# Kernel tuning notes

Measured on AMD Instinct MI355X. Metric: run time of the kernel, lower is better.

## Reference

```python
import jax, jax.numpy as jnp
import numpy as np

B, T, D, H = 4, 2048, 1024, 16
HD = D // H  # 64


def setup_inputs() -> dict:
    key = jax.random.key(0)
    ks = jax.random.split(key, 9)
    s = 1.0 / np.sqrt(D)
    return {
        "x": jax.random.normal(ks[0], (B, T, D), dtype=jnp.float32),
        "Wq": jax.random.normal(ks[1], (D, D), dtype=jnp.float32) * s,
        "bq": jnp.zeros((D,), dtype=jnp.float32),
        "Wk": jax.random.normal(ks[2], (D, D), dtype=jnp.float32) * s,
        "bk": jnp.zeros((D,), dtype=jnp.float32),
        "Wv": jax.random.normal(ks[3], (D, D), dtype=jnp.float32) * s,
        "bv": jnp.zeros((D,), dtype=jnp.float32),
        "Wo": jax.random.normal(ks[4], (D, D), dtype=jnp.float32) * s,
        "bo": jnp.zeros((D,), dtype=jnp.float32),
    }


def reference(x, Wq, bq, Wk, bk, Wv, bv, Wo, bo):
    Bx, Tx, C = x.shape
    # QKV projections -> (B, H, T, HD)
    q = (x @ Wq + bq).reshape(Bx, Tx, H, HD).transpose(0, 2, 1, 3)
    k = (x @ Wk + bk).reshape(Bx, Tx, H, HD).transpose(0, 2, 1, 3)
    v = (x @ Wv + bv).reshape(Bx, Tx, H, HD).transpose(0, 2, 1, 3)
    # scaled dot-product scores (B, H, T, T)
    scores = jnp.einsum("bhqd,bhkd->bhqk", q, k) / jnp.sqrt(jnp.float32(HD))
    causal = jnp.tril(jnp.ones((Tx, Tx), dtype=bool))
    scores = jnp.where(causal[None, None, :, :], scores, jnp.float32(-1e9))
    attn = jax.nn.softmax(scores, axis=-1)
    out = jnp.einsum("bhqk,bhkd->bhqd", attn, v)  # (B, H, T, HD)
    out = out.transpose(0, 2, 1, 3).reshape(Bx, Tx, C)
    return out @ Wo + bo
```

## Files before the change

### kernel.cpp

```cpp
#include <hip/hip_runtime.h>


#define B_  4
#define T_  2048
#define D_  1024
#define H_  16
#define HD_ 64
#define M_  (B_ * T_)

typedef __bf16 bf16x8 __attribute__((ext_vector_type(8)));
typedef float  floatx4 __attribute__((ext_vector_type(4)));

__device__ __forceinline__ unsigned short f2b(float f) {
  unsigned int u = __float_as_uint(f);
  unsigned int r = (u + 0x7fffu + ((u >> 16) & 1u)) >> 16;
  return (unsigned short)r;
}

__device__ __forceinline__ float fast_exp2(float x) {
#if __has_builtin(__builtin_amdgcn_exp2f)
  return __builtin_amdgcn_exp2f(x);
#else
  return exp2f(x);
#endif
}

__device__ __forceinline__ void async_ld16(const void* g, void* l) {
  __builtin_amdgcn_global_load_lds(
      (const __attribute__((address_space(1))) void*)g,
      (__attribute__((address_space(3))) void*)l, 16, 0, 0);
}


__global__ void cast_fp32_to_bf16(const float* __restrict__ in,
                                  unsigned short* __restrict__ out, int n) {
  int i = (blockIdx.x * 256 + threadIdx.x) * 4;
  if (i >= n) return;
  float4 v = *(const float4*)(in + i);
  ushort4 o;
  o.x = f2b(v.x); o.y = f2b(v.y); o.z = f2b(v.z); o.w = f2b(v.w);
  *(ushort4*)(out + i) = o;
}

__global__ void transpose_cast(const float* __restrict__ W0, const float* __restrict__ W1,
                               const float* __restrict__ W2, const float* __restrict__ W3,
                               unsigned short* __restrict__ O0, unsigned short* __restrict__ O1,
                               unsigned short* __restrict__ O2, unsigned short* __restrict__ O3) {
  __shared__ float tile[32][33];
  int z = blockIdx.z;
  const float* W = z == 0 ? W0 : z == 1 ? W1 : z == 2 ? W2 : W3;
  unsigned short* O = z == 0 ? O0 : z == 1 ? O1 : z == 2 ? O2 : O3;
  int n0 = blockIdx.x * 32, k0 = blockIdx.y * 32;
  int tx = threadIdx.x, ty = threadIdx.y;
#pragma unroll
  for (int i = 0; i < 4; ++i)
    tile[ty + i * 8][tx] = W[(size_t)(k0 + ty + i * 8) * D_ + n0 + tx];
  __syncthreads();
#pragma unroll
  for (int i = 0; i < 4; ++i)
    O[(size_t)(n0 + ty + i * 8) * D_ + k0 + tx] = f2b(tile[tx][ty + i * 8]);
}


__global__ __launch_bounds__(256, 2)
void gemm_qkv(const unsigned short* __restrict__ A,
              const unsigned short* __restrict__ Wt,
              const float* __restrict__ bq, const float* __restrict__ bk,
              const float* __restrict__ bv,
              unsigned short* __restrict__ Qo, unsigned short* __restrict__ Ko,
              unsigned short* __restrict__ Vo) {
  __shared__ __align__(16) unsigned short As[128 * 64];
  __shared__ __align__(16) unsigned short Bs[128 * 64];
  const int K = D_;

  const int tid = threadIdx.x;
  const int wave = tid >> 6, lane = tid & 63;
  const int quad = lane >> 4, l16 = lane & 15;
  const int m0 = blockIdx.y * 128, n0 = blockIdx.x * 128;
  const int wm = (wave >> 1) * 64, wn = (wave & 1) * 64;

  const int rsub = lane >> 3;
  const int csw = ((lane & 7) ^ rsub) * 8;
  const int rw = wave * 32;

  const unsigned short* Ag = A + (size_t)(m0 + rw + rsub) * K + csw;
  const unsigned short* Bg = Wt + (size_t)(n0 + rw + rsub) * K + csw;

  floatx4 acc[4][4] = {};

  for (int kt = 0; kt < K; kt += 64) {
#pragma unroll
    for (int j = 0; j < 4; ++j) {
      async_ld16(Ag + (size_t)(j * 8) * K + kt, &As[(rw + j * 8) * 64]);
      async_ld16(Bg + (size_t)(j * 8) * K + kt, &Bs[(rw + j * 8) * 64]);
    }
    __syncthreads();

#pragma unroll
    for (int kk = 0; kk < 2; ++kk) {
      bf16x8 a[4], b[4];
#pragma unroll
      for (int i = 0; i < 4; ++i) {
        const int ra = wm + i * 16 + l16;
        a[i] = *(const bf16x8*)&As[ra * 64 + (((kk * 4 + quad) ^ (ra & 7)) * 8)];
      }
#pragma unroll
      for (int i = 0; i < 4; ++i) {
        const int rb = wn + i * 16 + l16;
        b[i] = *(const bf16x8*)&Bs[rb * 64 + (((kk * 4 + quad) ^ (rb & 7)) * 8)];
      }
#pragma unroll
      for (int mi = 0; mi < 4; ++mi)
#pragma unroll
        for (int ni = 0; ni < 4; ++ni)
          acc[mi][ni] = __builtin_amdgcn_mfma_f32_16x16x32_bf16(
              a[mi], b[ni], acc[mi][ni], 0, 0, 0);
    }
    __syncthreads();
  }

  const int which = n0 >> 10;
  const float* bias = which == 0 ? bq : which == 1 ? bk : bv;
  unsigned short* Out = which == 0 ? Qo : which == 1 ? Ko : Vo;

#pragma unroll
  for (int mi = 0; mi < 4; ++mi) {
#pragma unroll
    for (int ni = 0; ni < 4; ++ni) {
#pragma unroll
      for (int r = 0; r < 4; ++r) {
        const int m = m0 + wm + mi * 16 + quad * 4 + r;
        const int n = n0 + wn + ni * 16 + l16;
        const float val = acc[mi][ni][r] + bias[n & 1023];
        const int b = m >> 11, t = m & (T_ - 1);
        const int nl = n & 1023;
        const int h = nl >> 6, d = nl & (HD_ - 1);
        size_t idx;
        if (which == 2) {
          const int tp = (t & ~63) | (((t & 15) << 2) | ((t >> 4) & 3));
          idx = ((size_t)(b * H_ + h) * HD_ + d) * T_ + tp;
        } else {
          idx = ((size_t)(b * H_ + h) * T_ + t) * HD_ + d;
        }
        Out[idx] = f2b(val);
      }
    }
  }
}


__global__ __launch_bounds__(256, 2)
void gemm_out(const unsigned short* __restrict__ A,
              const unsigned short* __restrict__ Bt,
              const float* __restrict__ bias,
              float* __restrict__ Cout, int N, int K) {
  __shared__ __align__(16) unsigned short As[128 * 64];
  __shared__ __align__(16) unsigned short Bs[128 * 64];

  const int tid = threadIdx.x;
  const int wave = tid >> 6, lane = tid & 63;
  const int quad = lane >> 4, l16 = lane & 15;
  const int m0 = blockIdx.y * 128, n0 = blockIdx.x * 128;
  const int wm = (wave >> 1) * 64, wn = (wave & 1) * 64;

  const int rsub = lane >> 3;
  const int csw = ((lane & 7) ^ rsub) * 8;
  const int rw = wave * 32;

  const unsigned short* Ag = A + (size_t)(m0 + rw + rsub) * K + csw;
  const unsigned short* Bg = Bt + (size_t)(n0 + rw + rsub) * K + csw;

  floatx4 acc[4][4] = {};

  for (int kt = 0; kt < K; kt += 64) {
#pragma unroll
    for (int j = 0; j < 4; ++j) {
      async_ld16(Ag + (size_t)(j * 8) * K + kt, &As[(rw + j * 8) * 64]);
      async_ld16(Bg + (size_t)(j * 8) * K + kt, &Bs[(rw + j * 8) * 64]);
    }
    __syncthreads();

#pragma unroll
    for (int kk = 0; kk < 2; ++kk) {
      bf16x8 a[4], b[4];
#pragma unroll
      for (int i = 0; i < 4; ++i) {
        const int ra = wm + i * 16 + l16;
        a[i] = *(const bf16x8*)&As[ra * 64 + (((kk * 4 + quad) ^ (ra & 7)) * 8)];
      }
#pragma unroll
      for (int i = 0; i < 4; ++i) {
        const int rb = wn + i * 16 + l16;
        b[i] = *(const bf16x8*)&Bs[rb * 64 + (((kk * 4 + quad) ^ (rb & 7)) * 8)];
      }
#pragma unroll
      for (int mi = 0; mi < 4; ++mi)
#pragma unroll
        for (int ni = 0; ni < 4; ++ni)
          acc[mi][ni] = __builtin_amdgcn_mfma_f32_16x16x32_bf16(
              a[mi], b[ni], acc[mi][ni], 0, 0, 0);
    }
    __syncthreads();
  }

#pragma unroll
  for (int mi = 0; mi < 4; ++mi)
#pragma unroll
    for (int ni = 0; ni < 4; ++ni)
#pragma unroll
      for (int r = 0; r < 4; ++r) {
        const int m = m0 + wm + mi * 16 + quad * 4 + r;
        const int n = n0 + wn + ni * 16 + l16;
        Cout[(size_t)m * N + n] = acc[mi][ni][r] + bias[n];
      }
}


#define PSTR 72

template <bool MASKED>
__device__ __forceinline__ void attn_chunk(
    int kbse, int qw, int quad, int l16,
    const unsigned short* __restrict__ Ks,
    const unsigned short* __restrict__ Vs,
    const bf16x8 (&aq)[2][2], floatx4 (&o)[2][4], floatx4 (&lacc)[2],
    unsigned short* __restrict__ pl0, unsigned short* __restrict__ pl1,
    bf16x8 vones) {
  const int sw = l16 & 7;

  bf16x8 kf0[4], kf1[4];
#pragma unroll
  for (int j = 0; j < 4; ++j) {
    const unsigned short* kr = &Ks[(j * 16 + l16) * HD_];
    kf0[j] = *(const bf16x8*)&kr[(quad ^ sw) * 8];
    kf1[j] = *(const bf16x8*)&kr[((quad + 4) ^ sw) * 8];
  }

  floatx4 s[2][4] = {};
#pragma unroll
  for (int qt = 0; qt < 2; ++qt)
#pragma unroll
    for (int j = 0; j < 4; ++j) {
      s[qt][j] = __builtin_amdgcn_mfma_f32_16x16x32_bf16(aq[qt][0], kf0[j], s[qt][j], 0, 0, 0);
      s[qt][j] = __builtin_amdgcn_mfma_f32_16x16x32_bf16(aq[qt][1], kf1[j], s[qt][j], 0, 0, 0);
    }

  bf16x8 vf0[4], vf1[4];
#pragma unroll
  for (int d4 = 0; d4 < 4; ++d4) {
    const unsigned short* vr = &Vs[(d4 * 16 + l16) * 64];
    vf0[d4] = *(const bf16x8*)&vr[(quad ^ sw) * 8];
    vf1[d4] = *(const bf16x8*)&vr[((quad + 4) ^ sw) * 8];
  }

  const float SL = 0.125f * 1.44269504f;
  const float CB = 8.0f * 1.44269504f;
#pragma unroll
  for (int qt = 0; qt < 2; ++qt) {
    unsigned short* pw = qt ? pl1 : pl0;
#pragma unroll
    for (int r = 0; r < 4; ++r) {
      float v0 = s[qt][0][r], v1 = s[qt][1][r], v2 = s[qt][2][r], v3 = s[qt][3][r];
      if (MASKED) {
        const int qrow = qw + qt * 16 + quad * 4 + r;
        if (kbse + l16 > qrow)      v0 = -1e30f;
        if (kbse + 16 + l16 > qrow) v1 = -1e30f;
        if (kbse + 32 + l16 > qrow) v2 = -1e30f;
        if (kbse + 48 + l16 > qrow) v3 = -1e30f;
      }
      const float p0 = fast_exp2(__builtin_fmaf(v0, SL, -CB));
      const float p1 = fast_exp2(__builtin_fmaf(v1, SL, -CB));
      const float p2 = fast_exp2(__builtin_fmaf(v2, SL, -CB));
      const float p3 = fast_exp2(__builtin_fmaf(v3, SL, -CB));
      uint2 pk;
      pk.x = __builtin_amdgcn_perm(__float_as_uint(p1), __float_as_uint(p0), 0x07060302u);
      pk.y = __builtin_amdgcn_perm(__float_as_uint(p3), __float_as_uint(p2), 0x07060302u);
      *(uint2*)&pw[(quad * 4 + r) * PSTR + 4 * l16] = pk;
    }
  }

#pragma unroll
  for (int qt = 0; qt < 2; ++qt) {
    const unsigned short* pw = qt ? pl1 : pl0;
    const bf16x8 pf0 = *(const bf16x8*)&pw[l16 * PSTR + quad * 8];
    const bf16x8 pf1 = *(const bf16x8*)&pw[l16 * PSTR + 32 + quad * 8];
    lacc[qt] = __builtin_amdgcn_mfma_f32_16x16x32_bf16(pf0, vones, lacc[qt], 0, 0, 0);
    lacc[qt] = __builtin_amdgcn_mfma_f32_16x16x32_bf16(pf1, vones, lacc[qt], 0, 0, 0);
#pragma unroll
    for (int d4 = 0; d4 < 4; ++d4) {
      o[qt][d4] = __builtin_amdgcn_mfma_f32_16x16x32_bf16(pf0, vf0[d4], o[qt][d4], 0, 0, 0);
      o[qt][d4] = __builtin_amdgcn_mfma_f32_16x16x32_bf16(pf1, vf1[d4], o[qt][d4], 0, 0, 0);
    }
  }
}

__global__ __launch_bounds__(256, 2)
void attn_kernel(const unsigned short* __restrict__ Q,
                 const unsigned short* __restrict__ K,
                 const unsigned short* __restrict__ Vp,
                 unsigned short* __restrict__ O) {
  __shared__ __align__(16) unsigned short Ks[64 * HD_];
  __shared__ __align__(16) unsigned short Vs[HD_ * 64];
  __shared__ unsigned short Pl[4][2][16 * PSTR];

  const int bidx = blockIdx.x;
  const int xcd = bidx & 7;
  const int t = bidx >> 3;
  const int j = t >> 5;
  const int slot = t & 31;
  const int bh_local = slot >> 2;
  const int v = slot & 3;
  const int k4 = (j == 0) ? v : (j == 1) ? 15 - v : (j == 2) ? v + 4 : 11 - v;
  const int bh = (xcd << 3) | bh_local;

  const int wave = threadIdx.x >> 6, lane = threadIdx.x & 63;
  const int quad = lane >> 4, l16 = lane & 15;
  const int tile = k4 * 4 + wave;
  const int qw = tile * 32;

  const unsigned short* Qb = Q + (size_t)bh * T_ * HD_;
  const unsigned short* Kb = K + (size_t)bh * T_ * HD_;
  const unsigned short* Vb = Vp + (size_t)bh * HD_ * T_;

  bf16x8 aq[2][2];
#pragma unroll
  for (int qt = 0; qt < 2; ++qt) {
    const unsigned short* qp = Qb + (size_t)(qw + qt * 16 + l16) * HD_;
    aq[qt][0] = *(const bf16x8*)(qp + quad * 8);
    aq[qt][1] = *(const bf16x8*)(qp + 32 + quad * 8);
  }

  union { unsigned short u[8]; bf16x8 v8; } ones;
#pragma unroll
  for (int i = 0; i < 8; ++i) ones.u[i] = 0x3F80;

  floatx4 o[2][4] = {};
  floatx4 lacc[2] = {};

  const int rsub = lane >> 3;
  const int csw = ((lane & 7) ^ rsub) * 8;
  const int rA = 8 * wave;
  const int rB = 8 * (wave + 4);

  const int my_nfull = tile >> 1;
  const int nit = 2 * k4 + 2;

  for (int kc = 0; kc < nit; ++kc) {
    const int kbse = kc * 64;
    if (kc) __syncthreads();
    async_ld16(Kb + (size_t)(kbse + rA + rsub) * HD_ + csw, &Ks[rA * HD_]);
    async_ld16(Kb + (size_t)(kbse + rB + rsub) * HD_ + csw, &Ks[rB * HD_]);
    async_ld16(Vb + (size_t)(rA + rsub) * T_ + kbse + csw, &Vs[rA * 64]);
    async_ld16(Vb + (size_t)(rB + rsub) * T_ + kbse + csw, &Vs[rB * 64]);
    __syncthreads();

    if (kc < my_nfull)
      attn_chunk<false>(kbse, qw, quad, l16, Ks, Vs, aq, o, lacc,
                        &Pl[wave][0][0], &Pl[wave][1][0], ones.v8);
    else if (kc == my_nfull)
      attn_chunk<true>(kbse, qw, quad, l16, Ks, Vs, aq, o, lacc,
                       &Pl[wave][0][0], &Pl[wave][1][0], ones.v8);
  }

  const int b = bh >> 4, h = bh & 15;
#pragma unroll
  for (int qt = 0; qt < 2; ++qt) {
#pragma unroll
    for (int r = 0; r < 4; ++r) {
      const float inv = 1.0f / lacc[qt][r];
      const int tt = qw + qt * 16 + quad * 4 + r;
      unsigned short* orow = O + (size_t)(b * T_ + tt) * D_ + h * HD_;
      orow[l16]      = f2b(o[qt][0][r] * inv);
      orow[16 + l16] = f2b(o[qt][1][r] * inv);
      orow[32 + l16] = f2b(o[qt][2][r] * inv);
      orow[48 + l16] = f2b(o[qt][3][r] * inv);
    }
  }
}


extern "C" void kernel_launch(void* const* d_in, const int* in_sizes, int n_in,
                              void* d_out, int out_size, void* d_ws, size_t ws_size,
                              hipStream_t stream) {
  const float* x  = (const float*)d_in[0];
  const float* Wq = (const float*)d_in[1];
  const float* bq = (const float*)d_in[2];
  const float* Wk = (const float*)d_in[3];
  const float* bk = (const float*)d_in[4];
  const float* Wv = (const float*)d_in[5];
  const float* bv = (const float*)d_in[6];
  const float* Wo = (const float*)d_in[7];
  const float* bo = (const float*)d_in[8];
  float* out = (float*)d_out;

  char* ws = (char*)d_ws;
  const size_t MB = 1u << 20;
  unsigned short* xb  = (unsigned short*)(ws);
  unsigned short* Wqt = (unsigned short*)(ws + 16 * MB);
  unsigned short* Wkt = (unsigned short*)(ws + 18 * MB);
  unsigned short* Wvt = (unsigned short*)(ws + 20 * MB);
  unsigned short* Wot = (unsigned short*)(ws + 22 * MB);
  unsigned short* Qb  = (unsigned short*)(ws + 24 * MB);
  unsigned short* Kb  = (unsigned short*)(ws + 40 * MB);
  unsigned short* Vtb = (unsigned short*)(ws + 56 * MB);
  unsigned short* Ob  = xb;

  cast_fp32_to_bf16<<<dim3(M_ * D_ / 1024), dim3(256), 0, stream>>>(x, xb, M_ * D_);
  transpose_cast<<<dim3(32, 32, 4), dim3(32, 8), 0, stream>>>(
      Wq, Wk, Wv, Wo, Wqt, Wkt, Wvt, Wot);

  gemm_qkv<<<dim3(24, M_ / 128), dim3(256), 0, stream>>>(
      xb, Wqt, bq, bk, bv, Qb, Kb, Vtb);

  attn_kernel<<<dim3(1024), dim3(256), 0, stream>>>(Qb, Kb, Vtb, Ob);

  gemm_out<<<dim3(D_ / 128, M_ / 128), dim3(256), 0, stream>>>(
      Ob, Wot, bo, out, D_, D_);
}
```

Baseline: 259.6 us.

## Overlap next K/V tile load with softmax and PV compute in attention

Splits the attention chunk into a QK/V-fragment-load phase and a softmax+PV phase. After K and V fragments are pulled into registers, the single shared buffer is released and the async load for the next tile is issued, so global loads overlap the softmax and PV work. This keeps a single LDS buffer but holds V fragments in registers longer, which adds register pressure. Barriers per iteration stay at two.

After: 264.4 us. About the same (+1.8%).

```diff
diff --git a/kernel.cpp b/kernel.cpp
--- a/kernel.cpp
+++ b/kernel.cpp
@@ -218,14 +218,12 @@
 
 #define PSTR 72
 
-template <bool MASKED>
-__device__ __forceinline__ void attn_chunk(
-    int kbse, int qw, int quad, int l16,
+__device__ __forceinline__ void attn_qk(
+    int quad, int l16,
     const unsigned short* __restrict__ Ks,
     const unsigned short* __restrict__ Vs,
-    const bf16x8 (&aq)[2][2], floatx4 (&o)[2][4], floatx4 (&lacc)[2],
-    unsigned short* __restrict__ pl0, unsigned short* __restrict__ pl1,
-    bf16x8 vones) {
+    const bf16x8 (&aq)[2][2], floatx4 (&s)[2][4],
+    bf16x8 (&vf0)[4], bf16x8 (&vf1)[4]) {
   const int sw = l16 & 7;
 
   bf16x8 kf0[4], kf1[4];
@@ -236,7 +234,6 @@
     kf1[j] = *(const bf16x8*)&kr[((quad + 4) ^ sw) * 8];
   }
 
-  floatx4 s[2][4] = {};
 #pragma unroll
   for (int qt = 0; qt < 2; ++qt)
 #pragma unroll
@@ -245,14 +242,21 @@
       s[qt][j] = __builtin_amdgcn_mfma_f32_16x16x32_bf16(aq[qt][1], kf1[j], s[qt][j], 0, 0, 0);
     }
 
-  bf16x8 vf0[4], vf1[4];
 #pragma unroll
   for (int d4 = 0; d4 < 4; ++d4) {
     const unsigned short* vr = &Vs[(d4 * 16 + l16) * 64];
     vf0[d4] = *(const bf16x8*)&vr[(quad ^ sw) * 8];
     vf1[d4] = *(const bf16x8*)&vr[((quad + 4) ^ sw) * 8];
   }
-
+}
+
+template <bool MASKED>
+__device__ __forceinline__ void attn_sm_pv(
+    int kbse, int qw, int quad, int l16,
+    floatx4 (&s)[2][4], const bf16x8 (&vf0)[4], const bf16x8 (&vf1)[4],
+    floatx4 (&o)[2][4], floatx4 (&lacc)[2],
+    unsigned short* __restrict__ pl0, unsigned short* __restrict__ pl1,
+    bf16x8 vones) {
   const float SL = 0.125f * 1.44269504f;
   const float CB = 8.0f * 1.44269504f;
 #pragma unroll
@@ -345,21 +349,40 @@
   const int my_nfull = tile >> 1;
   const int nit = 2 * k4 + 2;
 
+  async_ld16(Kb + (size_t)(rA + rsub) * HD_ + csw, &Ks[rA * HD_]);
+  async_ld16(Kb + (size_t)(rB + rsub) * HD_ + csw, &Ks[rB * HD_]);
+  async_ld16(Vb + (size_t)(rA + rsub) * T_ + csw, &Vs[rA * 64]);
+  async_ld16(Vb + (size_t)(rB + rsub) * T_ + csw, &Vs[rB * 64]);
+  __syncthreads();
+
   for (int kc = 0; kc < nit; ++kc) {
     const int kbse = kc * 64;
-    if (kc) __syncthreads();
-    async_ld16(Kb + (size_t)(kbse + rA + rsub) * HD_ + csw, &Ks[rA * HD_]);
-    async_ld16(Kb + (size_t)(kbse + rB + rsub) * HD_ + csw, &Ks[rB * HD_]);
-    async_ld16(Vb + (size_t)(rA + rsub) * T_ + kbse + csw, &Vs[rA * 64]);
-    async_ld16(Vb + (size_t)(rB + rsub) * T_ + kbse + csw, &Vs[rB * 64]);
+    const bool active = kc <= my_nfull;
+
+    floatx4 s[2][4] = {};
+    bf16x8 vf0[4], vf1[4];
+    if (active)
+      attn_qk(quad, l16, Ks, Vs, aq, s, vf0, vf1);
+
     __syncthreads();
 
+    if (kc + 1 < nit) {
+      const int kn = kbse + 64;
+      async_ld16(Kb + (size_t)(kn + rA + rsub) * HD_ + csw, &Ks[rA * HD_]);
+      async_ld16(Kb + (size_t)(kn + rB + rsub) * HD_ + csw, &Ks[rB * HD_]);
+      async_ld16(Vb + (size_t)(rA + rsub) * T_ + kn + csw, &Vs[rA * 64]);
+      async_ld16(Vb + (size_t)(rB + rsub) * T_ + kn + csw, &Vs[rB * 64]);
+    }
+
     if (kc < my_nfull)
-      attn_chunk<false>(kbse, qw, quad, l16, Ks, Vs, aq, o, lacc,
+      attn_sm_pv<false>(kbse, qw, quad, l16, s, vf0, vf1, o, lacc,
                         &Pl[wave][0][0], &Pl[wave][1][0], ones.v8);
     else if (kc == my_nfull)
-      attn_chunk<true>(kbse, qw, quad, l16, Ks, Vs, aq, o, lacc,
+      attn_sm_pv<true>(kbse, qw, quad, l16, s, vf0, vf1, o, lacc,
                        &Pl[wave][0][0], &Pl[wave][1][0], ones.v8);
+
+    if (kc + 1 < nit)
+      __syncthreads();
   }
 
   const int b = bh >> 4, h = bh & 15;
```

## Widen attention per-wave query tile to 64 rows and halve grid

Applied to the files above, without the earlier changes.

Each wave now processes 64 query rows (four 16-row subtiles) instead of 32, so each K/V chunk staged in shared memory is reused across twice as many queries. The grid halves to 512 blocks, and block-to-query-group mapping is redone with a paired heavy/light causal ordering for load balance. The main costs targeted are global K/V loads and barrier overhead per useful MFMA. In exchange, per-thread register pressure and per-wave P scratch space grow, and the causal diagonal chunk now wastes more masked work per wave. Fewer blocks also risks lower occupancy and weaker load balance across CUs.

Result: slower. 264.8 us (median of 2 runs) (+2.0%).

```diff
diff --git a/kernel.cpp b/kernel.cpp
--- a/kernel.cpp
+++ b/kernel.cpp
@@ -219,12 +219,12 @@
 #define PSTR 72
 
 template <bool MASKED>
-__device__ __forceinline__ void attn_chunk(
+__device__ __forceinline__ void attn_chunk64(
     int kbse, int qw, int quad, int l16,
     const unsigned short* __restrict__ Ks,
     const unsigned short* __restrict__ Vs,
-    const bf16x8 (&aq)[2][2], floatx4 (&o)[2][4], floatx4 (&lacc)[2],
-    unsigned short* __restrict__ pl0, unsigned short* __restrict__ pl1,
+    const bf16x8 (&aq)[4][2], floatx4 (&o)[4][4], floatx4 (&lacc)[4],
+    unsigned short* __restrict__ plw,
     bf16x8 vones) {
   const int sw = l16 & 7;
 
@@ -236,31 +236,21 @@
     kf1[j] = *(const bf16x8*)&kr[((quad + 4) ^ sw) * 8];
   }
 
-  floatx4 s[2][4] = {};
-#pragma unroll
-  for (int qt = 0; qt < 2; ++qt)
-#pragma unroll
-    for (int j = 0; j < 4; ++j) {
-      s[qt][j] = __builtin_amdgcn_mfma_f32_16x16x32_bf16(aq[qt][0], kf0[j], s[qt][j], 0, 0, 0);
-      s[qt][j] = __builtin_amdgcn_mfma_f32_16x16x32_bf16(aq[qt][1], kf1[j], s[qt][j], 0, 0, 0);
-    }
-
-  bf16x8 vf0[4], vf1[4];
-#pragma unroll
-  for (int d4 = 0; d4 < 4; ++d4) {
-    const unsigned short* vr = &Vs[(d4 * 16 + l16) * 64];
-    vf0[d4] = *(const bf16x8*)&vr[(quad ^ sw) * 8];
-    vf1[d4] = *(const bf16x8*)&vr[((quad + 4) ^ sw) * 8];
-  }
-
   const float SL = 0.125f * 1.44269504f;
   const float CB = 8.0f * 1.44269504f;
-#pragma unroll
-  for (int qt = 0; qt < 2; ++qt) {
-    unsigned short* pw = qt ? pl1 : pl0;
+
+#pragma unroll
+  for (int qt = 0; qt < 4; ++qt) {
+    floatx4 s[4] = {};
+#pragma unroll
+    for (int j = 0; j < 4; ++j) {
+      s[j] = __builtin_amdgcn_mfma_f32_16x16x32_bf16(aq[qt][0], kf0[j], s[j], 0, 0, 0);
+      s[j] = __builtin_amdgcn_mfma_f32_16x16x32_bf16(aq[qt][1], kf1[j], s[j], 0, 0, 0);
+    }
+    unsigned short* pw = plw + qt * (16 * PSTR);
 #pragma unroll
     for (int r = 0; r < 4; ++r) {
-      float v0 = s[qt][0][r], v1 = s[qt][1][r], v2 = s[qt][2][r], v3 = s[qt][3][r];
+      float v0 = s[0][r], v1 = s[1][r], v2 = s[2][r], v3 = s[3][r];
       if (MASKED) {
         const int qrow = qw + qt * 16 + quad * 4 + r;
         if (kbse + l16 > qrow)      v0 = -1e30f;
@@ -279,9 +269,17 @@
     }
   }
 
-#pragma unroll
-  for (int qt = 0; qt < 2; ++qt) {
-    const unsigned short* pw = qt ? pl1 : pl0;
+  bf16x8 vf0[4], vf1[4];
+#pragma unroll
+  for (int d4 = 0; d4 < 4; ++d4) {
+    const unsigned short* vr = &Vs[(d4 * 16 + l16) * 64];
+    vf0[d4] = *(const bf16x8*)&vr[(quad ^ sw) * 8];
+    vf1[d4] = *(const bf16x8*)&vr[((quad + 4) ^ sw) * 8];
+  }
+
+#pragma unroll
+  for (int qt = 0; qt < 4; ++qt) {
+    const unsigned short* pw = plw + qt * (16 * PSTR);
     const bf16x8 pf0 = *(const bf16x8*)&pw[l16 * PSTR + quad * 8];
     const bf16x8 pf1 = *(const bf16x8*)&pw[l16 * PSTR + 32 + quad * 8];
     lacc[qt] = __builtin_amdgcn_mfma_f32_16x16x32_bf16(pf0, vones, lacc[qt], 0, 0, 0);
@@ -301,30 +299,28 @@
                  unsigned short* __restrict__ O) {
   __shared__ __align__(16) unsigned short Ks[64 * HD_];
   __shared__ __align__(16) unsigned short Vs[HD_ * 64];
-  __shared__ unsigned short Pl[4][2][16 * PSTR];
+  __shared__ unsigned short Pl[4][4][16 * PSTR];
 
   const int bidx = blockIdx.x;
   const int xcd = bidx & 7;
-  const int t = bidx >> 3;
-  const int j = t >> 5;
-  const int slot = t & 31;
-  const int bh_local = slot >> 2;
-  const int v = slot & 3;
-  const int k4 = (j == 0) ? v : (j == 1) ? 15 - v : (j == 2) ? v + 4 : 11 - v;
+  const int i = bidx >> 3;
+  const int bh_local = i & 7;
+  const int g = i >> 3;
+  const int kg = (g < 4) ? g : 11 - g;
   const int bh = (xcd << 3) | bh_local;
 
   const int wave = threadIdx.x >> 6, lane = threadIdx.x & 63;
   const int quad = lane >> 4, l16 = lane & 15;
-  const int tile = k4 * 4 + wave;
-  const int qw = tile * 32;
+  const int tile = kg * 4 + wave;
+  const int qw = tile * 64;
 
   const unsigned short* Qb = Q + (size_t)bh * T_ * HD_;
   const unsigned short* Kb = K + (size_t)bh * T_ * HD_;
   const unsigned short* Vb = Vp + (size_t)bh * HD_ * T_;
 
-  bf16x8 aq[2][2];
-#pragma unroll
-  for (int qt = 0; qt < 2; ++qt) {
+  bf16x8 aq[4][2];
+#pragma unroll
+  for (int qt = 0; qt < 4; ++qt) {
     const unsigned short* qp = Qb + (size_t)(qw + qt * 16 + l16) * HD_;
     aq[qt][0] = *(const bf16x8*)(qp + quad * 8);
     aq[qt][1] = *(const bf16x8*)(qp + 32 + quad * 8);
@@ -332,18 +328,18 @@
 
   union { unsigned short u[8]; bf16x8 v8; } ones;
 #pragma unroll
-  for (int i = 0; i < 8; ++i) ones.u[i] = 0x3F80;
-
-  floatx4 o[2][4] = {};
-  floatx4 lacc[2] = {};
+  for (int i2 = 0; i2 < 8; ++i2) ones.u[i2] = 0x3F80;
+
+  floatx4 o[4][4] = {};
+  floatx4 lacc[4] = {};
 
   const int rsub = lane >> 3;
   const int csw = ((lane & 7) ^ rsub) * 8;
   const int rA = 8 * wave;
   const int rB = 8 * (wave + 4);
 
-  const int my_nfull = tile >> 1;
-  const int nit = 2 * k4 + 2;
+  const int my_nfull = tile;
+  const int nit = 4 * kg + 4;
 
   for (int kc = 0; kc < nit; ++kc) {
     const int kbse = kc * 64;
@@ -355,16 +351,16 @@
     __syncthreads();
 
     if (kc < my_nfull)
-      attn_chunk<false>(kbse, qw, quad, l16, Ks, Vs, aq, o, lacc,
-                        &Pl[wave][0][0], &Pl[wave][1][0], ones.v8);
+      attn_chunk64<false>(kbse, qw, quad, l16, Ks, Vs, aq, o, lacc,
+                          &Pl[wave][0][0], ones.v8);
     else if (kc == my_nfull)
-      attn_chunk<true>(kbse, qw, quad, l16, Ks, Vs, aq, o, lacc,
-                       &Pl[wave][0][0], &Pl[wave][1][0], ones.v8);
+      attn_chunk64<true>(kbse, qw, quad, l16, Ks, Vs, aq, o, lacc,
+                         &Pl[wave][0][0], ones.v8);
   }
 
   const int b = bh >> 4, h = bh & 15;
 #pragma unroll
-  for (int qt = 0; qt < 2; ++qt) {
+  for (int qt = 0; qt < 4; ++qt) {
 #pragma unroll
     for (int r = 0; r < 4; ++r) {
       const float inv = 1.0f / lacc[qt][r];
@@ -412,7 +408,7 @@
   gemm_qkv<<<dim3(24, M_ / 128), dim3(256), 0, stream>>>(
       xb, Wqt, bq, bk, bv, Qb, Kb, Vtb);
 
-  attn_kernel<<<dim3(1024), dim3(256), 0, stream>>>(Qb, Kb, Vtb, Ob);
+  attn_kernel<<<dim3(512), dim3(256), 0, stream>>>(Qb, Kb, Vtb, Ob);
 
   gemm_out<<<dim3(D_ / 128, M_ / 128), dim3(256), 0, stream>>>(
       Ob, Wot, bo, out, D_, D_);
```
